# Performance work log

Measured on AMD Instinct MI355X. Metric: run time of the kernel, lower is better.

## Reference

```python
import jax, jax.numpy as jnp
import numpy as np
from jax.ops import segment_sum

N_NODES = 50000
N_EDGES = 800000
IN_CH, HIDDEN, OUT_CH = 64, 128, 64


def _glorot(key, fan_in, fan_out):
    lim = np.sqrt(6.0 / (fan_in + fan_out)).astype(np.float32)
    return jax.random.uniform(key, (fan_in, fan_out), jnp.float32, -lim, lim)


def setup_inputs() -> dict:
    key = jax.random.key(0)
    ks = jax.random.split(key, 10)
    x = jax.random.normal(ks[0], (N_NODES, IN_CH), jnp.float32)
    edge_index = jax.random.randint(ks[1], (2, N_EDGES), 0, N_NODES, jnp.int64)
    return {
        "x": x,
        "edge_index": edge_index,
        # GINConv1 MLP: Linear(in,hidden) -> ReLU -> Linear(hidden,hidden)
        "W1": _glorot(ks[2], IN_CH, HIDDEN),
        "b1": jnp.zeros((HIDDEN,), jnp.float32),
        "W2": _glorot(ks[3], HIDDEN, HIDDEN),
        "b2": jnp.zeros((HIDDEN,), jnp.float32),
        "eps1": jnp.zeros((), jnp.float32),
        # GINConv2 MLP: Linear(hidden,hidden) -> ReLU -> Linear(hidden,out)
        "W3": _glorot(ks[4], HIDDEN, HIDDEN),
        "b3": jnp.zeros((HIDDEN,), jnp.float32),
        "W4": _glorot(ks[5], HIDDEN, OUT_CH),
        "b4": jnp.zeros((OUT_CH,), jnp.float32),
        "eps2": jnp.zeros((), jnp.float32),
    }


def _gin_conv(x, src, dst, eps, Wa, ba, Wb, bb):
    # message = x[src]; aggregate = scatter-add at dst (sum aggregation)
    agg = segment_sum(x[src], dst, num_segments=N_NODES)  # [N, C]
    h = (1.0 + eps) * x + agg
    h = jax.nn.relu(h @ Wa + ba)
    return h @ Wb + bb


def reference(x, edge_index, W1, b1, W2, b2, eps1, W3, b3, W4, b4, eps2):
    src, dst = edge_index[0], edge_index[1]
    h1 = jax.nn.relu(_gin_conv(x, src, dst, eps1, W1, b1, W2, b2))
    h2 = _gin_conv(h1, src, dst, eps2, W3, b3, W4, b4)
    return h2
```

## Files before the change

### kernel.cpp

```cpp
#include <hip/hip_runtime.h>

#define N_NODES 50000
#define N_EDGES 800000
#define IN_CH 64
#define HIDDEN 128
#define OUT_CH 64
#define CAP 64
#define BINS 196
#define CHUNK 3125
#define LCAP 48
#define SEGCAP 4608

typedef unsigned short ushort_t;
typedef unsigned int uint_t;
typedef __attribute__((ext_vector_type(8))) short short8;
typedef __attribute__((ext_vector_type(4))) float f32x4;

__device__ __forceinline__ float bits2f(unsigned int u16) {
    union { unsigned int i; float f; } v;
    v.i = (u16 & 0xFFFFu) << 16;
    return v.f;
}

__device__ __forceinline__ ushort_t f2bits(float f) {
    union { float f; unsigned int i; } v;
    v.f = f;
    unsigned int x = v.i;
    if ((x & 0x7F800000u) == 0x7F800000u) return (ushort_t)(x >> 16);
    unsigned int r = (x + 0x7FFFu + ((x >> 16) & 1u)) >> 16;
    return (ushort_t)r;
}

__device__ __forceinline__ uint_t pack2(float x, float y) {
    return (uint_t)f2bits(x) | ((uint_t)f2bits(y) << 16);
}

__global__ __launch_bounds__(256) void binA_prep(const int* __restrict__ ei,
                                                 int* __restrict__ gcur,
                                                 uint_t* __restrict__ seg,
                                                 const float* __restrict__ x,
                                                 uint_t* __restrict__ xu,
                                                 const float* __restrict__ W1, ushort_t* __restrict__ pW1,
                                                 const float* __restrict__ W2, ushort_t* __restrict__ pW2,
                                                 const float* __restrict__ W3, ushort_t* __restrict__ pW3,
                                                 const float* __restrict__ W4, ushort_t* __restrict__ pW4) {
    __shared__ uint_t lbin[BINS][LCAP];
    __shared__ int lcnt[BINS];
    __shared__ int lbase[BINS];
    int blk = blockIdx.x;
    int t = threadIdx.x;
    if (blk < 256) {
        for (int i = t; i < BINS; i += 256) lcnt[i] = 0;
        __syncthreads();
        int e0 = blk * CHUNK;
        int e1 = e0 + CHUNK; if (e1 > N_EDGES) e1 = N_EDGES;
        for (int e = e0 + t; e < e1; e += 256) {
            int src = ei[e];
            int dst = ei[N_EDGES + e];
            int bin = dst >> 8;
            uint_t rec = ((uint_t)src << 16) | (uint_t)(dst & 255);
            int pos = atomicAdd(&lcnt[bin], 1);
            if (pos < LCAP) {
                lbin[bin][pos] = rec;
            } else {
                int gp = atomicAdd(&gcur[bin], 1);
                if (gp < SEGCAP) seg[(size_t)bin * SEGCAP + gp] = rec;
            }
        }
        __syncthreads();
        for (int i = t; i < BINS; i += 256) {
            int c = lcnt[i]; if (c > LCAP) c = LCAP;
            lbase[i] = atomicAdd(&gcur[i], c);
        }
        __syncthreads();
        int wv = t >> 6, ln = t & 63;
        for (int i = wv; i < BINS; i += 4) {
            int c = lcnt[i]; if (c > LCAP) c = LCAP;
            int base = lbase[i];
            for (int j = ln; j < c; j += 64)
                seg[(size_t)i * SEGCAP + base + j] = lbin[i][j];
        }
    } else if (blk < 448) {
        int b = blk - 256;
        const float* W; ushort_t* o; int K, C, b0;
        if (b < 32)       { W = W1; o = pW1; K = IN_CH;  C = HIDDEN; b0 = 0; }
        else if (b < 96)  { W = W2; o = pW2; K = HIDDEN; C = HIDDEN; b0 = 32; }
        else if (b < 160) { W = W3; o = pW3; K = HIDDEN; C = HIDDEN; b0 = 96; }
        else              { W = W4; o = pW4; K = HIDDEN; C = OUT_CH; b0 = 160; }
        int tid = (b - b0) * 256 + t;
        int j = tid & 7;
        int l = (tid >> 3) & 63;
        int rest = tid >> 9;
        int KC = K >> 5;
        int kc = rest % KC;
        int nt = rest / KC;
        int k = kc * 32 + (l >> 4) * 8 + j;
        int n = nt * 16 + (l & 15);
        o[tid] = f2bits(W[(size_t)k * C + n]);
    } else {
        int i = (blk - 448) * 256 + t;
        if (i < N_NODES * IN_CH / 2) {
            float2 v = ((const float2*)x)[i];
            xu[i] = pack2(v.x, v.y);
        }
    }
}

__global__ __launch_bounds__(256) void binB(const uint_t* __restrict__ seg,
                                            const int* __restrict__ gcur,
                                            int* __restrict__ cnt,
                                            ushort_t* __restrict__ bucket) {
    __shared__ ushort_t lb[256 * CAP];
    __shared__ int lc[256];
    int b = blockIdx.x;
    int t = threadIdx.x;
    lc[t] = 0;
    __syncthreads();
    int c = gcur[b]; if (c > SEGCAP) c = SEGCAP;
    const uint_t* s = seg + (size_t)b * SEGCAP;
    for (int i = t; i < c; i += 256) {
        uint_t rec = s[i];
        int ldst = rec & 255;
        int pos = atomicAdd(&lc[ldst], 1);
        if (pos < CAP) lb[ldst * CAP + pos] = (ushort_t)(rec >> 16);
    }
    __syncthreads();
    int n0 = b * 256;
    int nvalid = N_NODES - n0; if (nvalid > 256) nvalid = 256;
    uint4* gb = (uint4*)(bucket + (size_t)n0 * CAP);
    const uint4* lbv = (const uint4*)lb;
    int total = nvalid * (CAP / 8);
    for (int i = t; i < total; i += 256) gb[i] = lbv[i];
    if (t < nvalid) cnt[n0 + t] = lc[t];
}

__global__ __launch_bounds__(256) void gather1(const uint_t* __restrict__ xu,
                                               const int* __restrict__ cnt,
                                               const ushort_t* __restrict__ bucket,
                                               const float* __restrict__ eps1,
                                               uint_t* __restrict__ agg1b) {
    int tid = threadIdx.x;
    int li = tid & 31;
    int n = blockIdx.x * 8 + (tid >> 5);
    uint_t v = xu[(size_t)n * 32 + li];
    float se = 1.0f + eps1[0];
    float s0 = se * bits2f(v), s1 = se * bits2f(v >> 16);
    float A0 = 0.f, A1 = 0.f, B0 = 0.f, B1 = 0.f, C0 = 0.f, C1 = 0.f, D0 = 0.f, D1 = 0.f;
    float E0 = 0.f, E1 = 0.f, F0 = 0.f, F1 = 0.f, G0 = 0.f, G1 = 0.f, H0 = 0.f, H1 = 0.f;
    int cn = cnt[n]; if (cn > CAP) cn = CAP;
    const ushort_t* bk = bucket + (size_t)n * CAP;
    int i = 0;
    for (; i + 7 < cn; i += 8) {
        uint4 p = *(const uint4*)(bk + i);
        uint_t u0 = xu[(size_t)(p.x & 0xFFFFu) * 32 + li];
        uint_t u1 = xu[(size_t)(p.x >> 16) * 32 + li];
        uint_t u2 = xu[(size_t)(p.y & 0xFFFFu) * 32 + li];
        uint_t u3 = xu[(size_t)(p.y >> 16) * 32 + li];
        uint_t u4 = xu[(size_t)(p.z & 0xFFFFu) * 32 + li];
        uint_t u5 = xu[(size_t)(p.z >> 16) * 32 + li];
        uint_t u6 = xu[(size_t)(p.w & 0xFFFFu) * 32 + li];
        uint_t u7 = xu[(size_t)(p.w >> 16) * 32 + li];
        A0 += bits2f(u0); A1 += bits2f(u0 >> 16);
        B0 += bits2f(u1); B1 += bits2f(u1 >> 16);
        C0 += bits2f(u2); C1 += bits2f(u2 >> 16);
        D0 += bits2f(u3); D1 += bits2f(u3 >> 16);
        E0 += bits2f(u4); E1 += bits2f(u4 >> 16);
        F0 += bits2f(u5); F1 += bits2f(u5 >> 16);
        G0 += bits2f(u6); G1 += bits2f(u6 >> 16);
        H0 += bits2f(u7); H1 += bits2f(u7 >> 16);
    }
    for (; i + 3 < cn; i += 4) {
        ushort4 e4 = *(const ushort4*)(bk + i);
        uint_t u0 = xu[(size_t)e4.x * 32 + li];
        uint_t u1 = xu[(size_t)e4.y * 32 + li];
        uint_t u2 = xu[(size_t)e4.z * 32 + li];
        uint_t u3 = xu[(size_t)e4.w * 32 + li];
        A0 += bits2f(u0); A1 += bits2f(u0 >> 16);
        B0 += bits2f(u1); B1 += bits2f(u1 >> 16);
        C0 += bits2f(u2); C1 += bits2f(u2 >> 16);
        D0 += bits2f(u3); D1 += bits2f(u3 >> 16);
    }
    for (; i < cn; i++) {
        uint_t u = xu[(size_t)bk[i] * 32 + li];
        s0 += bits2f(u); s1 += bits2f(u >> 16);
    }
    agg1b[(size_t)n * 32 + li] =
        pack2(s0 + ((A0 + B0) + (C0 + D0)) + ((E0 + F0) + (G0 + H0)),
              s1 + ((A1 + B1) + (C1 + D1)) + ((E1 + F1) + (G1 + H1)));
}

__global__ __launch_bounds__(256) void gather2(const ushort_t* __restrict__ h1,
                                               const int* __restrict__ cnt,
                                               const ushort_t* __restrict__ bucket,
                                               const float* __restrict__ eps2,
                                               uint_t* __restrict__ agg2b) {
    int lane = threadIdx.x & 63;
    int n = blockIdx.x * 4 + (threadIdx.x >> 6);
    const uint_t* h1u = (const uint_t*)h1;
    uint_t v = h1u[(size_t)n * 64 + lane];
    float se = 1.0f + eps2[0];
    float s0 = se * bits2f(v), s1 = se * bits2f(v >> 16);
    float A0 = 0.f, A1 = 0.f, B0 = 0.f, B1 = 0.f, C0 = 0.f, C1 = 0.f, D0 = 0.f, D1 = 0.f;
    float E0 = 0.f, E1 = 0.f, F0 = 0.f, F1 = 0.f, G0 = 0.f, G1 = 0.f, H0 = 0.f, H1 = 0.f;
    int cn = cnt[n]; if (cn > CAP) cn = CAP;
    const ushort_t* bk = bucket + (size_t)n * CAP;
    int i = 0;
    for (; i + 7 < cn; i += 8) {
        uint4 p = *(const uint4*)(bk + i);
        uint_t u0 = h1u[(size_t)(p.x & 0xFFFFu) * 64 + lane];
        uint_t u1 = h1u[(size_t)(p.x >> 16) * 64 + lane];
        uint_t u2 = h1u[(size_t)(p.y & 0xFFFFu) * 64 + lane];
        uint_t u3 = h1u[(size_t)(p.y >> 16) * 64 + lane];
        uint_t u4 = h1u[(size_t)(p.z & 0xFFFFu) * 64 + lane];
        uint_t u5 = h1u[(size_t)(p.z >> 16) * 64 + lane];
        uint_t u6 = h1u[(size_t)(p.w & 0xFFFFu) * 64 + lane];
        uint_t u7 = h1u[(size_t)(p.w >> 16) * 64 + lane];
        A0 += bits2f(u0); A1 += bits2f(u0 >> 16);
        B0 += bits2f(u1); B1 += bits2f(u1 >> 16);
        C0 += bits2f(u2); C1 += bits2f(u2 >> 16);
        D0 += bits2f(u3); D1 += bits2f(u3 >> 16);
        E0 += bits2f(u4); E1 += bits2f(u4 >> 16);
        F0 += bits2f(u5); F1 += bits2f(u5 >> 16);
        G0 += bits2f(u6); G1 += bits2f(u6 >> 16);
        H0 += bits2f(u7); H1 += bits2f(u7 >> 16);
    }
    for (; i + 3 < cn; i += 4) {
        ushort4 e4 = *(const ushort4*)(bk + i);
        uint_t u0 = h1u[(size_t)e4.x * 64 + lane];
        uint_t u1 = h1u[(size_t)e4.y * 64 + lane];
        uint_t u2 = h1u[(size_t)e4.z * 64 + lane];
        uint_t u3 = h1u[(size_t)e4.w * 64 + lane];
        A0 += bits2f(u0); A1 += bits2f(u0 >> 16);
        B0 += bits2f(u1); B1 += bits2f(u1 >> 16);
        C0 += bits2f(u2); C1 += bits2f(u2 >> 16);
        D0 += bits2f(u3); D1 += bits2f(u3 >> 16);
    }
    for (; i < cn; i++) {
        uint_t u = h1u[(size_t)bk[i] * 64 + lane];
        s0 += bits2f(u); s1 += bits2f(u >> 16);
    }
    agg2b[(size_t)n * 64 + lane] =
        pack2(s0 + ((A0 + B0) + (C0 + D0)) + ((E0 + F0) + (G0 + H0)),
              s1 + ((A1 + B1) + (C1 + D1)) + ((E1 + F1) + (G1 + H1)));
}

#define TPAD 136

__global__ __launch_bounds__(256) void mlp1(const ushort_t* __restrict__ agg1b,
                                            const ushort_t* __restrict__ pW1,
                                            const float* __restrict__ b1,
                                            const ushort_t* __restrict__ pW2,
                                            const float* __restrict__ b2,
                                            ushort_t* __restrict__ h1) {
    __shared__ __align__(16) ushort_t t[64][TPAD];
    int w = threadIdx.x >> 6;
    int l = threadIdx.x & 63;
    int q = l >> 4;
    int c = l & 15;
    int m0 = blockIdx.x * 64 + w * 16;
    int node = m0 + c;
    int nc = node < N_NODES ? node : 0;
    short8 a0 = *(const short8*)(agg1b + (size_t)nc * IN_CH + q * 8);
    short8 a1 = *(const short8*)(agg1b + (size_t)nc * IN_CH + 32 + q * 8);
#pragma unroll
    for (int nt = 0; nt < 8; nt++) {
        float bb = b1[nt * 16 + c];
        f32x4 acc = {bb, bb, bb, bb};
        short8 bf0 = *(const short8*)(pW1 + (size_t)((nt * 2 + 0) * 64 + l) * 8);
        short8 bf1 = *(const short8*)(pW1 + (size_t)((nt * 2 + 1) * 64 + l) * 8);
        acc = __builtin_amdgcn_mfma_f32_16x16x32_bf16(a0, bf0, acc, 0, 0, 0);
        acc = __builtin_amdgcn_mfma_f32_16x16x32_bf16(a1, bf1, acc, 0, 0, 0);
#pragma unroll
        for (int r = 0; r < 4; r++)
            t[w * 16 + q * 4 + r][nt * 16 + c] = f2bits(fmaxf(acc[r], 0.0f));
    }
    __syncthreads();
    short8 A[4];
#pragma unroll
    for (int kc = 0; kc < 4; kc++)
        A[kc] = *(const short8*)&t[w * 16 + c][kc * 32 + q * 8];
#pragma unroll
    for (int nt = 0; nt < 8; nt++) {
        float bb = b2[nt * 16 + c];
        f32x4 acc = {bb, bb, bb, bb};
#pragma unroll
        for (int kc = 0; kc < 4; kc++) {
            short8 bf = *(const short8*)(pW2 + (size_t)((nt * 4 + kc) * 64 + l) * 8);
            acc = __builtin_amdgcn_mfma_f32_16x16x32_bf16(A[kc], bf, acc, 0, 0, 0);
        }
#pragma unroll
        for (int r = 0; r < 4; r++) {
            int rr = m0 + q * 4 + r;
            if (rr < N_NODES)
                h1[(size_t)rr * HIDDEN + nt * 16 + c] = f2bits(fmaxf(acc[r], 0.0f));
        }
    }
}

__global__ __launch_bounds__(256) void mlp2(const ushort_t* __restrict__ agg2b,
                                            const ushort_t* __restrict__ pW3,
                                            const float* __restrict__ b3,
                                            const ushort_t* __restrict__ pW4,
                                            const float* __restrict__ b4,
                                            float* __restrict__ out) {
    __shared__ __align__(16) ushort_t t[64][TPAD];
    int w = threadIdx.x >> 6;
    int l = threadIdx.x & 63;
    int q = l >> 4;
    int c = l & 15;
    int m0 = blockIdx.x * 64 + w * 16;
    int node = m0 + c;
    int nc = node < N_NODES ? node : 0;
    short8 A[4];
#pragma unroll
    for (int kc = 0; kc < 4; kc++)
        A[kc] = *(const short8*)(agg2b + (size_t)nc * HIDDEN + kc * 32 + q * 8);
#pragma unroll
    for (int nt = 0; nt < 8; nt++) {
        float bb = b3[nt * 16 + c];
        f32x4 acc = {bb, bb, bb, bb};
#pragma unroll
        for (int kc = 0; kc < 4; kc++) {
            short8 bf = *(const short8*)(pW3 + (size_t)((nt * 4 + kc) * 64 + l) * 8);
            acc = __builtin_amdgcn_mfma_f32_16x16x32_bf16(A[kc], bf, acc, 0, 0, 0);
        }
#pragma unroll
        for (int r = 0; r < 4; r++)
            t[w * 16 + q * 4 + r][nt * 16 + c] = f2bits(fmaxf(acc[r], 0.0f));
    }
    __syncthreads();
    short8 B[4];
#pragma unroll
    for (int kc = 0; kc < 4; kc++)
        B[kc] = *(const short8*)&t[w * 16 + c][kc * 32 + q * 8];
#pragma unroll
    for (int nt = 0; nt < 4; nt++) {
        float bb = b4[nt * 16 + c];
        f32x4 acc = {bb, bb, bb, bb};
#pragma unroll
        for (int kc = 0; kc < 4; kc++) {
            short8 bf = *(const short8*)(pW4 + (size_t)((nt * 4 + kc) * 64 + l) * 8);
            acc = __builtin_amdgcn_mfma_f32_16x16x32_bf16(B[kc], bf, acc, 0, 0, 0);
        }
#pragma unroll
        for (int r = 0; r < 4; r++) {
            int rr = m0 + q * 4 + r;
            if (rr < N_NODES)
                out[(size_t)rr * OUT_CH + nt * 16 + c] = acc[r];
        }
    }
}

extern "C" void kernel_launch(void* const* d_in, const int* in_sizes, int n_in,
                              void* d_out, int out_size, void* d_ws, size_t ws_size,
                              hipStream_t stream) {
    const float* x    = (const float*)d_in[0];
    const int*   ei   = (const int*)d_in[1];
    const float* W1   = (const float*)d_in[2];
    const float* b1   = (const float*)d_in[3];
    const float* W2   = (const float*)d_in[4];
    const float* b2   = (const float*)d_in[5];
    const float* eps1 = (const float*)d_in[6];
    const float* W3   = (const float*)d_in[7];
    const float* b3   = (const float*)d_in[8];
    const float* W4   = (const float*)d_in[9];
    const float* b4   = (const float*)d_in[10];
    const float* eps2 = (const float*)d_in[11];
    float* out = (float*)d_out;

    ushort_t* wsU = (ushort_t*)d_ws;
    ushort_t* agg2b = wsU;
    uint_t*   xb    = (uint_t*)wsU;
    ushort_t* h1    = wsU + (size_t)6400000;
    ushort_t* agg1b = wsU + (size_t)12800000;
    ushort_t* pW    = wsU + (size_t)16000000;
    ushort_t* pW1 = pW;
    ushort_t* pW2 = pW + 8192;
    ushort_t* pW3 = pW + 24576;
    ushort_t* pW4 = pW + 40960;
    int* cnt         = (int*)(wsU + (size_t)16049152);
    ushort_t* bucket = (ushort_t*)(cnt + N_NODES);
    int* gcur        = (int*)(bucket + (size_t)N_NODES * CAP);
    uint_t* seg      = (uint_t*)(gcur + 256);

    hipMemsetAsync(gcur, 0, BINS * sizeof(int), stream);
    int cvtBlocks = (N_NODES * IN_CH / 2 + 255) / 256;
    binA_prep<<<448 + cvtBlocks, 256, 0, stream>>>(
        ei, gcur, seg, x, xb, W1, pW1, W2, pW2, W3, pW3, W4, pW4);
    binB<<<BINS, 256, 0, stream>>>(seg, gcur, cnt, bucket);

    gather1<<<N_NODES / 8, 256, 0, stream>>>(xb, cnt, bucket, eps1, (uint_t*)agg1b);
    mlp1<<<(N_NODES + 63) / 64, 256, 0, stream>>>(agg1b, pW1, b1, pW2, b2, h1);

    gather2<<<N_NODES / 4, 256, 0, stream>>>(h1, cnt, bucket, eps2, (uint_t*)agg2b);
    mlp2<<<(N_NODES + 63) / 64, 256, 0, stream>>>(agg2b, pW3, b3, pW4, b4, out);
}
```

Measured before the change: 185.3 us.

## Fuse neighbor gather into MLP kernels via shared-memory staging per 64-node tile

Merges each gather kernel with its following MLP kernel: each block aggregates neighbor features for 64 nodes into LDS, then runs the MFMA MLP from LDS. This removes the agg1b/agg2b global round trips and two kernel launches. In exchange the gather phase now has far fewer blocks (782 vs 6250/12500), each looping serially over 8 or 16 nodes per wave group. That cuts the latency hiding for the random neighbor loads and may lower occupancy because of the added LDS use.

```diff
diff --git a/kernel.cpp b/kernel.cpp
--- a/kernel.cpp
+++ b/kernel.cpp
@@ -134,134 +134,80 @@
     if (t < nvalid) cnt[n0 + t] = lc[t];
 }
 
-__global__ __launch_bounds__(256) void gather1(const uint_t* __restrict__ xu,
-                                               const int* __restrict__ cnt,
-                                               const ushort_t* __restrict__ bucket,
-                                               const float* __restrict__ eps1,
-                                               uint_t* __restrict__ agg1b) {
+#define TPAD 136
+
+__global__ __launch_bounds__(256) void layer1(const uint_t* __restrict__ xu,
+                                              const int* __restrict__ cnt,
+                                              const ushort_t* __restrict__ bucket,
+                                              const float* __restrict__ eps1,
+                                              const ushort_t* __restrict__ pW1,
+                                              const float* __restrict__ b1,
+                                              const ushort_t* __restrict__ pW2,
+                                              const float* __restrict__ b2,
+                                              ushort_t* __restrict__ h1) {
+    __shared__ __align__(16) ushort_t t[64][TPAD];
     int tid = threadIdx.x;
-    int li = tid & 31;
-    int n = blockIdx.x * 8 + (tid >> 5);
-    uint_t v = xu[(size_t)n * 32 + li];
+    int m0 = blockIdx.x * 64;
+    int g = tid >> 5, li = tid & 31;
     float se = 1.0f + eps1[0];
-    float s0 = se * bits2f(v), s1 = se * bits2f(v >> 16);
-    float A0 = 0.f, A1 = 0.f, B0 = 0.f, B1 = 0.f, C0 = 0.f, C1 = 0.f, D0 = 0.f, D1 = 0.f;
-    float E0 = 0.f, E1 = 0.f, F0 = 0.f, F1 = 0.f, G0 = 0.f, G1 = 0.f, H0 = 0.f, H1 = 0.f;
-    int cn = cnt[n]; if (cn > CAP) cn = CAP;
-    const ushort_t* bk = bucket + (size_t)n * CAP;
-    int i = 0;
-    for (; i + 7 < cn; i += 8) {
-        uint4 p = *(const uint4*)(bk + i);
-        uint_t u0 = xu[(size_t)(p.x & 0xFFFFu) * 32 + li];
-        uint_t u1 = xu[(size_t)(p.x >> 16) * 32 + li];
-        uint_t u2 = xu[(size_t)(p.y & 0xFFFFu) * 32 + li];
-        uint_t u3 = xu[(size_t)(p.y >> 16) * 32 + li];
-        uint_t u4 = xu[(size_t)(p.z & 0xFFFFu) * 32 + li];
-        uint_t u5 = xu[(size_t)(p.z >> 16) * 32 + li];
-        uint_t u6 = xu[(size_t)(p.w & 0xFFFFu) * 32 + li];
-        uint_t u7 = xu[(size_t)(p.w >> 16) * 32 + li];
-        A0 += bits2f(u0); A1 += bits2f(u0 >> 16);
-        B0 += bits2f(u1); B1 += bits2f(u1 >> 16);
-        C0 += bits2f(u2); C1 += bits2f(u2 >> 16);
-        D0 += bits2f(u3); D1 += bits2f(u3 >> 16);
-        E0 += bits2f(u4); E1 += bits2f(u4 >> 16);
-        F0 += bits2f(u5); F1 += bits2f(u5 >> 16);
-        G0 += bits2f(u6); G1 += bits2f(u6 >> 16);
-        H0 += bits2f(u7); H1 += bits2f(u7 >> 16);
-    }
-    for (; i + 3 < cn; i += 4) {
-        ushort4 e4 = *(const ushort4*)(bk + i);
-        uint_t u0 = xu[(size_t)e4.x * 32 + li];
-        uint_t u1 = xu[(size_t)e4.y * 32 + li];
-        uint_t u2 = xu[(size_t)e4.z * 32 + li];
-        uint_t u3 = xu[(size_t)e4.w * 32 + li];
-        A0 += bits2f(u0); A1 += bits2f(u0 >> 16);
-        B0 += bits2f(u1); B1 += bits2f(u1 >> 16);
-        C0 += bits2f(u2); C1 += bits2f(u2 >> 16);
-        D0 += bits2f(u3); D1 += bits2f(u3 >> 16);
-    }
-    for (; i < cn; i++) {
-        uint_t u = xu[(size_t)bk[i] * 32 + li];
-        s0 += bits2f(u); s1 += bits2f(u >> 16);
-    }
-    agg1b[(size_t)n * 32 + li] =
-        pack2(s0 + ((A0 + B0) + (C0 + D0)) + ((E0 + F0) + (G0 + H0)),
-              s1 + ((A1 + B1) + (C1 + D1)) + ((E1 + F1) + (G1 + H1)));
-}
-
-__global__ __launch_bounds__(256) void gather2(const ushort_t* __restrict__ h1,
-                                               const int* __restrict__ cnt,
-                                               const ushort_t* __restrict__ bucket,
-                                               const float* __restrict__ eps2,
-                                               uint_t* __restrict__ agg2b) {
-    int lane = threadIdx.x & 63;
-    int n = blockIdx.x * 4 + (threadIdx.x >> 6);
-    const uint_t* h1u = (const uint_t*)h1;
-    uint_t v = h1u[(size_t)n * 64 + lane];
-    float se = 1.0f + eps2[0];
-    float s0 = se * bits2f(v), s1 = se * bits2f(v >> 16);
-    float A0 = 0.f, A1 = 0.f, B0 = 0.f, B1 = 0.f, C0 = 0.f, C1 = 0.f, D0 = 0.f, D1 = 0.f;
-    float E0 = 0.f, E1 = 0.f, F0 = 0.f, F1 = 0.f, G0 = 0.f, G1 = 0.f, H0 = 0.f, H1 = 0.f;
-    int cn = cnt[n]; if (cn > CAP) cn = CAP;
-    const ushort_t* bk = bucket + (size_t)n * CAP;
-    int i = 0;
-    for (; i + 7 < cn; i += 8) {
-        uint4 p = *(const uint4*)(bk + i);
-        uint_t u0 = h1u[(size_t)(p.x & 0xFFFFu) * 64 + lane];
-        uint_t u1 = h1u[(size_t)(p.x >> 16) * 64 + lane];
-        uint_t u2 = h1u[(size_t)(p.y & 0xFFFFu) * 64 + lane];
-        uint_t u3 = h1u[(size_t)(p.y >> 16) * 64 + lane];
-        uint_t u4 = h1u[(size_t)(p.z & 0xFFFFu) * 64 + lane];
-        uint_t u5 = h1u[(size_t)(p.z >> 16) * 64 + lane];
-        uint_t u6 = h1u[(size_t)(p.w & 0xFFFFu) * 64 + lane];
-        uint_t u7 = h1u[(size_t)(p.w >> 16) * 64 + lane];
-        A0 += bits2f(u0); A1 += bits2f(u0 >> 16);
-        B0 += bits2f(u1); B1 += bits2f(u1 >> 16);
-        C0 += bits2f(u2); C1 += bits2f(u2 >> 16);
-        D0 += bits2f(u3); D1 += bits2f(u3 >> 16);
-        E0 += bits2f(u4); E1 += bits2f(u4 >> 16);
-        F0 += bits2f(u5); F1 += bits2f(u5 >> 16);
-        G0 += bits2f(u6); G1 += bits2f(u6 >> 16);
-        H0 += bits2f(u7); H1 += bits2f(u7 >> 16);
-    }
-    for (; i + 3 < cn; i += 4) {
-        ushort4 e4 = *(const ushort4*)(bk + i);
-        uint_t u0 = h1u[(size_t)e4.x * 64 + lane];
-        uint_t u1 = h1u[(size_t)e4.y * 64 + lane];
-        uint_t u2 = h1u[(size_t)e4.z * 64 + lane];
-        uint_t u3 = h1u[(size_t)e4.w * 64 + lane];
-        A0 += bits2f(u0); A1 += bits2f(u0 >> 16);
-        B0 += bits2f(u1); B1 += bits2f(u1 >> 16);
-        C0 += bits2f(u2); C1 += bits2f(u2 >> 16);
-        D0 += bits2f(u3); D1 += bits2f(u3 >> 16);
-    }
-    for (; i < cn; i++) {
-        uint_t u = h1u[(size_t)bk[i] * 64 + lane];
-        s0 += bits2f(u); s1 += bits2f(u >> 16);
-    }
-    agg2b[(size_t)n * 64 + lane] =
-        pack2(s0 + ((A0 + B0) + (C0 + D0)) + ((E0 + F0) + (G0 + H0)),
-              s1 + ((A1 + B1) + (C1 + D1)) + ((E1 + F1) + (G1 + H1)));
-}
-
-#define TPAD 136
-
-__global__ __launch_bounds__(256) void mlp1(const ushort_t* __restrict__ agg1b,
-                                            const ushort_t* __restrict__ pW1,
-                                            const float* __restrict__ b1,
-                                            const ushort_t* __restrict__ pW2,
-                                            const float* __restrict__ b2,
-                                            ushort_t* __restrict__ h1) {
-    __shared__ __align__(16) ushort_t t[64][TPAD];
-    int w = threadIdx.x >> 6;
-    int l = threadIdx.x & 63;
+    for (int j = 0; j < 8; j++) {
+        int n = m0 + g * 8 + j;
+        float r0 = 0.f, r1 = 0.f;
+        if (n < N_NODES) {
+            uint_t v = xu[(size_t)n * 32 + li];
+            float s0 = se * bits2f(v), s1 = se * bits2f(v >> 16);
+            float A0 = 0.f, A1 = 0.f, B0 = 0.f, B1 = 0.f, C0 = 0.f, C1 = 0.f, D0 = 0.f, D1 = 0.f;
+            float E0 = 0.f, E1 = 0.f, F0 = 0.f, F1 = 0.f, G0 = 0.f, G1 = 0.f, H0 = 0.f, H1 = 0.f;
+            int cn = cnt[n]; if (cn > CAP) cn = CAP;
+            const ushort_t* bk = bucket + (size_t)n * CAP;
+            int i = 0;
+            for (; i + 7 < cn; i += 8) {
+                uint4 p = *(const uint4*)(bk + i);
+                uint_t u0 = xu[(size_t)(p.x & 0xFFFFu) * 32 + li];
+                uint_t u1 = xu[(size_t)(p.x >> 16) * 32 + li];
+                uint_t u2 = xu[(size_t)(p.y & 0xFFFFu) * 32 + li];
+                uint_t u3 = xu[(size_t)(p.y >> 16) * 32 + li];
+                uint_t u4 = xu[(size_t)(p.z & 0xFFFFu) * 32 + li];
+                uint_t u5 = xu[(size_t)(p.z >> 16) * 32 + li];
+                uint_t u6 = xu[(size_t)(p.w & 0xFFFFu) * 32 + li];
+                uint_t u7 = xu[(size_t)(p.w >> 16) * 32 + li];
+                A0 += bits2f(u0); A1 += bits2f(u0 >> 16);
+                B0 += bits2f(u1); B1 += bits2f(u1 >> 16);
+                C0 += bits2f(u2); C1 += bits2f(u2 >> 16);
+                D0 += bits2f(u3); D1 += bits2f(u3 >> 16);
+                E0 += bits2f(u4); E1 += bits2f(u4 >> 16);
+                F0 += bits2f(u5); F1 += bits2f(u5 >> 16);
+                G0 += bits2f(u6); G1 += bits2f(u6 >> 16);
+                H0 += bits2f(u7); H1 += bits2f(u7 >> 16);
+            }
+            for (; i + 3 < cn; i += 4) {
+                ushort4 e4 = *(const ushort4*)(bk + i);
+                uint_t u0 = xu[(size_t)e4.x * 32 + li];
+                uint_t u1 = xu[(size_t)e4.y * 32 + li];
+                uint_t u2 = xu[(size_t)e4.z * 32 + li];
+                uint_t u3 = xu[(size_t)e4.w * 32 + li];
+                A0 += bits2f(u0); A1 += bits2f(u0 >> 16);
+                B0 += bits2f(u1); B1 += bits2f(u1 >> 16);
+                C0 += bits2f(u2); C1 += bits2f(u2 >> 16);
+                D0 += bits2f(u3); D1 += bits2f(u3 >> 16);
+            }
+            for (; i < cn; i++) {
+                uint_t u = xu[(size_t)bk[i] * 32 + li];
+                s0 += bits2f(u); s1 += bits2f(u >> 16);
+            }
+            r0 = s0 + ((A0 + B0) + (C0 + D0)) + ((E0 + F0) + (G0 + H0));
+            r1 = s1 + ((A1 + B1) + (C1 + D1)) + ((E1 + F1) + (G1 + H1));
+        }
+        ((uint_t*)&t[g * 8 + j][0])[li] = pack2(r0, r1);
+    }
+    __syncthreads();
+    int w = tid >> 6;
+    int l = tid & 63;
     int q = l >> 4;
     int c = l & 15;
-    int m0 = blockIdx.x * 64 + w * 16;
-    int node = m0 + c;
-    int nc = node < N_NODES ? node : 0;
-    short8 a0 = *(const short8*)(agg1b + (size_t)nc * IN_CH + q * 8);
-    short8 a1 = *(const short8*)(agg1b + (size_t)nc * IN_CH + 32 + q * 8);
+    short8 a0 = *(const short8*)&t[w * 16 + c][q * 8];
+    short8 a1 = *(const short8*)&t[w * 16 + c][32 + q * 8];
+    __syncthreads();
 #pragma unroll
     for (int nt = 0; nt < 8; nt++) {
         float bb = b1[nt * 16 + c];
@@ -290,31 +236,88 @@
         }
 #pragma unroll
         for (int r = 0; r < 4; r++) {
-            int rr = m0 + q * 4 + r;
+            int rr = m0 + w * 16 + q * 4 + r;
             if (rr < N_NODES)
                 h1[(size_t)rr * HIDDEN + nt * 16 + c] = f2bits(fmaxf(acc[r], 0.0f));
         }
     }
 }
 
-__global__ __launch_bounds__(256) void mlp2(const ushort_t* __restrict__ agg2b,
-                                            const ushort_t* __restrict__ pW3,
-                                            const float* __restrict__ b3,
-                                            const ushort_t* __restrict__ pW4,
-                                            const float* __restrict__ b4,
-                                            float* __restrict__ out) {
+__global__ __launch_bounds__(256) void layer2(const ushort_t* __restrict__ h1,
+                                              const int* __restrict__ cnt,
+                                              const ushort_t* __restrict__ bucket,
+                                              const float* __restrict__ eps2,
+                                              const ushort_t* __restrict__ pW3,
+                                              const float* __restrict__ b3,
+                                              const ushort_t* __restrict__ pW4,
+                                              const float* __restrict__ b4,
+                                              float* __restrict__ out) {
     __shared__ __align__(16) ushort_t t[64][TPAD];
-    int w = threadIdx.x >> 6;
-    int l = threadIdx.x & 63;
+    int tid = threadIdx.x;
+    int m0 = blockIdx.x * 64;
+    int wv = tid >> 6, lane = tid & 63;
+    const uint_t* h1u = (const uint_t*)h1;
+    float se = 1.0f + eps2[0];
+    for (int j = 0; j < 16; j++) {
+        int n = m0 + wv * 16 + j;
+        float r0 = 0.f, r1 = 0.f;
+        if (n < N_NODES) {
+            uint_t v = h1u[(size_t)n * 64 + lane];
+            float s0 = se * bits2f(v), s1 = se * bits2f(v >> 16);
+            float A0 = 0.f, A1 = 0.f, B0 = 0.f, B1 = 0.f, C0 = 0.f, C1 = 0.f, D0 = 0.f, D1 = 0.f;
+            float E0 = 0.f, E1 = 0.f, F0 = 0.f, F1 = 0.f, G0 = 0.f, G1 = 0.f, H0 = 0.f, H1 = 0.f;
+            int cn = cnt[n]; if (cn > CAP) cn = CAP;
+            const ushort_t* bk = bucket + (size_t)n * CAP;
+            int i = 0;
+            for (; i + 7 < cn; i += 8) {
+                uint4 p = *(const uint4*)(bk + i);
+                uint_t u0 = h1u[(size_t)(p.x & 0xFFFFu) * 64 + lane];
+                uint_t u1 = h1u[(size_t)(p.x >> 16) * 64 + lane];
+                uint_t u2 = h1u[(size_t)(p.y & 0xFFFFu) * 64 + lane];
+                uint_t u3 = h1u[(size_t)(p.y >> 16) * 64 + lane];
+                uint_t u4 = h1u[(size_t)(p.z & 0xFFFFu) * 64 + lane];
+                uint_t u5 = h1u[(size_t)(p.z >> 16) * 64 + lane];
+                uint_t u6 = h1u[(size_t)(p.w & 0xFFFFu) * 64 + lane];
+                uint_t u7 = h1u[(size_t)(p.w >> 16) * 64 + lane];
+                A0 += bits2f(u0); A1 += bits2f(u0 >> 16);
+                B0 += bits2f(u1); B1 += bits2f(u1 >> 16);
+                C0 += bits2f(u2); C1 += bits2f(u2 >> 16);
+                D0 += bits2f(u3); D1 += bits2f(u3 >> 16);
+                E0 += bits2f(u4); E1 += bits2f(u4 >> 16);
+                F0 += bits2f(u5); F1 += bits2f(u5 >> 16);
+                G0 += bits2f(u6); G1 += bits2f(u6 >> 16);
+                H0 += bits2f(u7); H1 += bits2f(u7 >> 16);
+            }
+            for (; i + 3 < cn; i += 4) {
+                ushort4 e4 = *(const ushort4*)(bk + i);
+                uint_t u0 = h1u[(size_t)e4.x * 64 + lane];
+                uint_t u1 = h1u[(size_t)e4.y * 64 + lane];
+                uint_t u2 = h1u[(size_t)e4.z * 64 + lane];
+                uint_t u3 = h1u[(size_t)e4.w * 64 + lane];
+                A0 += bits2f(u0); A1 += bits2f(u0 >> 16);
+                B0 += bits2f(u1); B1 += bits2f(u1 >> 16);
+                C0 += bits2f(u2); C1 += bits2f(u2 >> 16);
+                D0 += bits2f(u3); D1 += bits2f(u3 >> 16);
+            }
+            for (; i < cn; i++) {
+                uint_t u = h1u[(size_t)bk[i] * 64 + lane];
+                s0 += bits2f(u); s1 += bits2f(u >> 16);
+            }
+            r0 = s0 + ((A0 + B0) + (C0 + D0)) + ((E0 + F0) + (G0 + H0));
+            r1 = s1 + ((A1 + B1) + (C1 + D1)) + ((E1 + F1) + (G1 + H1));
+        }
+        ((uint_t*)&t[wv * 16 + j][0])[lane] = pack2(r0, r1);
+    }
+    __syncthreads();
+    int w = tid >> 6;
+    int l = tid & 63;
     int q = l >> 4;
     int c = l & 15;
-    int m0 = blockIdx.x * 64 + w * 16;
-    int node = m0 + c;
-    int nc = node < N_NODES ? node : 0;
     short8 A[4];
 #pragma unroll
     for (int kc = 0; kc < 4; kc++)
-        A[kc] = *(const short8*)(agg2b + (size_t)nc * HIDDEN + kc * 32 + q * 8);
+        A[kc] = *(const short8*)&t[w * 16 + c][kc * 32 + q * 8];
+    __syncthreads();
 #pragma unroll
     for (int nt = 0; nt < 8; nt++) {
         float bb = b3[nt * 16 + c];
@@ -344,7 +347,7 @@
         }
 #pragma unroll
         for (int r = 0; r < 4; r++) {
-            int rr = m0 + q * 4 + r;
+            int rr = m0 + w * 16 + q * 4 + r;
             if (rr < N_NODES)
                 out[(size_t)rr * OUT_CH + nt * 16 + c] = acc[r];
         }
@@ -369,10 +372,8 @@
     float* out = (float*)d_out;
 
     ushort_t* wsU = (ushort_t*)d_ws;
-    ushort_t* agg2b = wsU;
     uint_t*   xb    = (uint_t*)wsU;
     ushort_t* h1    = wsU + (size_t)6400000;
-    ushort_t* agg1b = wsU + (size_t)12800000;
     ushort_t* pW    = wsU + (size_t)16000000;
     ushort_t* pW1 = pW;
     ushort_t* pW2 = pW + 8192;
@@ -389,9 +390,6 @@
         ei, gcur, seg, x, xb, W1, pW1, W2, pW2, W3, pW3, W4, pW4);
     binB<<<BINS, 256, 0, stream>>>(seg, gcur, cnt, bucket);
 
-    gather1<<<N_NODES / 8, 256, 0, stream>>>(xb, cnt, bucket, eps1, (uint_t*)agg1b);
-    mlp1<<<(N_NODES + 63) / 64, 256, 0, stream>>>(agg1b, pW1, b1, pW2, b2, h1);
-
-    gather2<<<N_NODES / 4, 256, 0, stream>>>(h1, cnt, bucket, eps2, (uint_t*)agg2b);
-    mlp2<<<(N_NODES + 63) / 64, 256, 0, stream>>>(agg2b, pW3, b3, pW4, b4, out);
-}
+    layer1<<<(N_NODES + 63) / 64, 256, 0, stream>>>(xb, cnt, bucket, eps1, pW1, b1, pW2, b2, h1);
+    layer2<<<(N_NODES + 63) / 64, 256, 0, stream>>>(h1, cnt, bucket, eps2, pW3, b3, pW4, b4, out);
+}
```

Result: slower. 208.3 us (+12.4%).

## Split neighbor gathers into feature-column slices across multiple launches

Applied to the files above, without the earlier changes.

Replaces the two gather kernels with one templated kernel in which each node's row is handled by 16 lanes covering a 64-byte column slice. The kernel is launched once per slice: twice for layer 1 and four times for layer 2. The aim is to shrink the working set of the gathered feature table per pass so random row reads hit cache better. It also adds a 16-wide unrolled inner loop for more memory-level parallelism. In exchange it re-reads the bucket indices and counts on every pass, adds extra launch overhead, and each gathered access is now a 64-byte fragment.

```diff
diff --git a/kernel.cpp b/kernel.cpp
--- a/kernel.cpp
+++ b/kernel.cpp
@@ -134,32 +134,43 @@
     if (t < nvalid) cnt[n0 + t] = lc[t];
 }
 
-__global__ __launch_bounds__(256) void gather1(const uint_t* __restrict__ xu,
+template<int SU>
+__global__ __launch_bounds__(256) void gatherS(const uint_t* __restrict__ rows,
                                                const int* __restrict__ cnt,
                                                const ushort_t* __restrict__ bucket,
-                                               const float* __restrict__ eps1,
-                                               uint_t* __restrict__ agg1b) {
+                                               const float* __restrict__ epsp,
+                                               uint_t* __restrict__ aggout,
+                                               int slice) {
     int tid = threadIdx.x;
-    int li = tid & 31;
-    int n = blockIdx.x * 8 + (tid >> 5);
-    uint_t v = xu[(size_t)n * 32 + li];
-    float se = 1.0f + eps1[0];
+    int li = (tid & 15) + slice * 16;
+    int n = blockIdx.x * 16 + (tid >> 4);
+    uint_t v = rows[(size_t)n * SU + li];
+    float se = 1.0f + epsp[0];
     float s0 = se * bits2f(v), s1 = se * bits2f(v >> 16);
     float A0 = 0.f, A1 = 0.f, B0 = 0.f, B1 = 0.f, C0 = 0.f, C1 = 0.f, D0 = 0.f, D1 = 0.f;
     float E0 = 0.f, E1 = 0.f, F0 = 0.f, F1 = 0.f, G0 = 0.f, G1 = 0.f, H0 = 0.f, H1 = 0.f;
     int cn = cnt[n]; if (cn > CAP) cn = CAP;
     const ushort_t* bk = bucket + (size_t)n * CAP;
     int i = 0;
-    for (; i + 7 < cn; i += 8) {
-        uint4 p = *(const uint4*)(bk + i);
-        uint_t u0 = xu[(size_t)(p.x & 0xFFFFu) * 32 + li];
-        uint_t u1 = xu[(size_t)(p.x >> 16) * 32 + li];
-        uint_t u2 = xu[(size_t)(p.y & 0xFFFFu) * 32 + li];
-        uint_t u3 = xu[(size_t)(p.y >> 16) * 32 + li];
-        uint_t u4 = xu[(size_t)(p.z & 0xFFFFu) * 32 + li];
-        uint_t u5 = xu[(size_t)(p.z >> 16) * 32 + li];
-        uint_t u6 = xu[(size_t)(p.w & 0xFFFFu) * 32 + li];
-        uint_t u7 = xu[(size_t)(p.w >> 16) * 32 + li];
+    for (; i + 15 < cn; i += 16) {
+        uint4 p  = *(const uint4*)(bk + i);
+        uint4 pp = *(const uint4*)(bk + i + 8);
+        uint_t u0 = rows[(size_t)(p.x & 0xFFFFu) * SU + li];
+        uint_t u1 = rows[(size_t)(p.x >> 16) * SU + li];
+        uint_t u2 = rows[(size_t)(p.y & 0xFFFFu) * SU + li];
+        uint_t u3 = rows[(size_t)(p.y >> 16) * SU + li];
+        uint_t u4 = rows[(size_t)(p.z & 0xFFFFu) * SU + li];
+        uint_t u5 = rows[(size_t)(p.z >> 16) * SU + li];
+        uint_t u6 = rows[(size_t)(p.w & 0xFFFFu) * SU + li];
+        uint_t u7 = rows[(size_t)(p.w >> 16) * SU + li];
+        uint_t u8 = rows[(size_t)(pp.x & 0xFFFFu) * SU + li];
+        uint_t u9 = rows[(size_t)(pp.x >> 16) * SU + li];
+        uint_t uA = rows[(size_t)(pp.y & 0xFFFFu) * SU + li];
+        uint_t uB = rows[(size_t)(pp.y >> 16) * SU + li];
+        uint_t uC = rows[(size_t)(pp.z & 0xFFFFu) * SU + li];
+        uint_t uD = rows[(size_t)(pp.z >> 16) * SU + li];
+        uint_t uE = rows[(size_t)(pp.w & 0xFFFFu) * SU + li];
+        uint_t uF = rows[(size_t)(pp.w >> 16) * SU + li];
         A0 += bits2f(u0); A1 += bits2f(u0 >> 16);
         B0 += bits2f(u1); B1 += bits2f(u1 >> 16);
         C0 += bits2f(u2); C1 += bits2f(u2 >> 16);
@@ -168,53 +179,25 @@
         F0 += bits2f(u5); F1 += bits2f(u5 >> 16);
         G0 += bits2f(u6); G1 += bits2f(u6 >> 16);
         H0 += bits2f(u7); H1 += bits2f(u7 >> 16);
-    }
-    for (; i + 3 < cn; i += 4) {
-        ushort4 e4 = *(const ushort4*)(bk + i);
-        uint_t u0 = xu[(size_t)e4.x * 32 + li];
-        uint_t u1 = xu[(size_t)e4.y * 32 + li];
-        uint_t u2 = xu[(size_t)e4.z * 32 + li];
-        uint_t u3 = xu[(size_t)e4.w * 32 + li];
-        A0 += bits2f(u0); A1 += bits2f(u0 >> 16);
-        B0 += bits2f(u1); B1 += bits2f(u1 >> 16);
-        C0 += bits2f(u2); C1 += bits2f(u2 >> 16);
-        D0 += bits2f(u3); D1 += bits2f(u3 >> 16);
-    }
-    for (; i < cn; i++) {
-        uint_t u = xu[(size_t)bk[i] * 32 + li];
-        s0 += bits2f(u); s1 += bits2f(u >> 16);
-    }
-    agg1b[(size_t)n * 32 + li] =
-        pack2(s0 + ((A0 + B0) + (C0 + D0)) + ((E0 + F0) + (G0 + H0)),
-              s1 + ((A1 + B1) + (C1 + D1)) + ((E1 + F1) + (G1 + H1)));
-}
-
-__global__ __launch_bounds__(256) void gather2(const ushort_t* __restrict__ h1,
-                                               const int* __restrict__ cnt,
-                                               const ushort_t* __restrict__ bucket,
-                                               const float* __restrict__ eps2,
-                                               uint_t* __restrict__ agg2b) {
-    int lane = threadIdx.x & 63;
-    int n = blockIdx.x * 4 + (threadIdx.x >> 6);
-    const uint_t* h1u = (const uint_t*)h1;
-    uint_t v = h1u[(size_t)n * 64 + lane];
-    float se = 1.0f + eps2[0];
-    float s0 = se * bits2f(v), s1 = se * bits2f(v >> 16);
-    float A0 = 0.f, A1 = 0.f, B0 = 0.f, B1 = 0.f, C0 = 0.f, C1 = 0.f, D0 = 0.f, D1 = 0.f;
-    float E0 = 0.f, E1 = 0.f, F0 = 0.f, F1 = 0.f, G0 = 0.f, G1 = 0.f, H0 = 0.f, H1 = 0.f;
-    int cn = cnt[n]; if (cn > CAP) cn = CAP;
-    const ushort_t* bk = bucket + (size_t)n * CAP;
-    int i = 0;
+        A0 += bits2f(u8); A1 += bits2f(u8 >> 16);
+        B0 += bits2f(u9); B1 += bits2f(u9 >> 16);
+        C0 += bits2f(uA); C1 += bits2f(uA >> 16);
+        D0 += bits2f(uB); D1 += bits2f(uB >> 16);
+        E0 += bits2f(uC); E1 += bits2f(uC >> 16);
+        F0 += bits2f(uD); F1 += bits2f(uD >> 16);
+        G0 += bits2f(uE); G1 += bits2f(uE >> 16);
+        H0 += bits2f(uF); H1 += bits2f(uF >> 16);
+    }
     for (; i + 7 < cn; i += 8) {
         uint4 p = *(const uint4*)(bk + i);
-        uint_t u0 = h1u[(size_t)(p.x & 0xFFFFu) * 64 + lane];
-        uint_t u1 = h1u[(size_t)(p.x >> 16) * 64 + lane];
-        uint_t u2 = h1u[(size_t)(p.y & 0xFFFFu) * 64 + lane];
-        uint_t u3 = h1u[(size_t)(p.y >> 16) * 64 + lane];
-        uint_t u4 = h1u[(size_t)(p.z & 0xFFFFu) * 64 + lane];
-        uint_t u5 = h1u[(size_t)(p.z >> 16) * 64 + lane];
-        uint_t u6 = h1u[(size_t)(p.w & 0xFFFFu) * 64 + lane];
-        uint_t u7 = h1u[(size_t)(p.w >> 16) * 64 + lane];
+        uint_t u0 = rows[(size_t)(p.x & 0xFFFFu) * SU + li];
+        uint_t u1 = rows[(size_t)(p.x >> 16) * SU + li];
+        uint_t u2 = rows[(size_t)(p.y & 0xFFFFu) * SU + li];
+        uint_t u3 = rows[(size_t)(p.y >> 16) * SU + li];
+        uint_t u4 = rows[(size_t)(p.z & 0xFFFFu) * SU + li];
+        uint_t u5 = rows[(size_t)(p.z >> 16) * SU + li];
+        uint_t u6 = rows[(size_t)(p.w & 0xFFFFu) * SU + li];
+        uint_t u7 = rows[(size_t)(p.w >> 16) * SU + li];
         A0 += bits2f(u0); A1 += bits2f(u0 >> 16);
         B0 += bits2f(u1); B1 += bits2f(u1 >> 16);
         C0 += bits2f(u2); C1 += bits2f(u2 >> 16);
@@ -226,20 +209,20 @@
     }
     for (; i + 3 < cn; i += 4) {
         ushort4 e4 = *(const ushort4*)(bk + i);
-        uint_t u0 = h1u[(size_t)e4.x * 64 + lane];
-        uint_t u1 = h1u[(size_t)e4.y * 64 + lane];
-        uint_t u2 = h1u[(size_t)e4.z * 64 + lane];
-        uint_t u3 = h1u[(size_t)e4.w * 64 + lane];
+        uint_t u0 = rows[(size_t)e4.x * SU + li];
+        uint_t u1 = rows[(size_t)e4.y * SU + li];
+        uint_t u2 = rows[(size_t)e4.z * SU + li];
+        uint_t u3 = rows[(size_t)e4.w * SU + li];
         A0 += bits2f(u0); A1 += bits2f(u0 >> 16);
         B0 += bits2f(u1); B1 += bits2f(u1 >> 16);
         C0 += bits2f(u2); C1 += bits2f(u2 >> 16);
         D0 += bits2f(u3); D1 += bits2f(u3 >> 16);
     }
     for (; i < cn; i++) {
-        uint_t u = h1u[(size_t)bk[i] * 64 + lane];
+        uint_t u = rows[(size_t)bk[i] * SU + li];
         s0 += bits2f(u); s1 += bits2f(u >> 16);
     }
-    agg2b[(size_t)n * 64 + lane] =
+    aggout[(size_t)n * SU + li] =
         pack2(s0 + ((A0 + B0) + (C0 + D0)) + ((E0 + F0) + (G0 + H0)),
               s1 + ((A1 + B1) + (C1 + D1)) + ((E1 + F1) + (G1 + H1)));
 }
@@ -389,9 +372,14 @@
         ei, gcur, seg, x, xb, W1, pW1, W2, pW2, W3, pW3, W4, pW4);
     binB<<<BINS, 256, 0, stream>>>(seg, gcur, cnt, bucket);
 
-    gather1<<<N_NODES / 8, 256, 0, stream>>>(xb, cnt, bucket, eps1, (uint_t*)agg1b);
+    gatherS<32><<<N_NODES / 16, 256, 0, stream>>>(xb, cnt, bucket, eps1, (uint_t*)agg1b, 0);
+    gatherS<32><<<N_NODES / 16, 256, 0, stream>>>(xb, cnt, bucket, eps1, (uint_t*)agg1b, 1);
     mlp1<<<(N_NODES + 63) / 64, 256, 0, stream>>>(agg1b, pW1, b1, pW2, b2, h1);
 
-    gather2<<<N_NODES / 4, 256, 0, stream>>>(h1, cnt, bucket, eps2, (uint_t*)agg2b);
+    const uint_t* h1u = (const uint_t*)h1;
+    gatherS<64><<<N_NODES / 16, 256, 0, stream>>>(h1u, cnt, bucket, eps2, (uint_t*)agg2b, 0);
+    gatherS<64><<<N_NODES / 16, 256, 0, stream>>>(h1u, cnt, bucket, eps2, (uint_t*)agg2b, 1);
+    gatherS<64><<<N_NODES / 16, 256, 0, stream>>>(h1u, cnt, bucket, eps2, (uint_t*)agg2b, 2);
+    gatherS<64><<<N_NODES / 16, 256, 0, stream>>>(h1u, cnt, bucket, eps2, (uint_t*)agg2b, 3);
     mlp2<<<(N_NODES + 63) / 64, 256, 0, stream>>>(agg2b, pW3, b3, pW4, b4, out);
 }
```

Result: slower. 222.8 us (+20.2%).
